# Kernel tuning notes

Hardware: AMD Instinct MI355X
Metric: run time of the kernel (lower is better)

The kernel has to match this reference:

```python
import jax, jax.numpy as jnp
import numpy as np

B, T, D, H, NC = 128, 784, 1, 512, 10


def setup_inputs() -> dict:
    key = jax.random.key(0)
    ks = jax.random.split(key, 8)
    x = jax.random.normal(ks[0], (B, T, D), dtype=jnp.float32)
    # UR-LSTM gate weights: chunks [f, r, u, o] each of size H
    Wx = jax.random.normal(ks[1], (D, 4 * H), dtype=jnp.float32) / np.sqrt(D)
    Wh = jax.random.normal(ks[2], (H, 4 * H), dtype=jnp.float32) / np.sqrt(H)
    b = jnp.zeros((4 * H,), dtype=jnp.float32)
    W1 = jax.random.normal(ks[3], (H * T, 256), dtype=jnp.float32) / np.sqrt(H * T)
    b1 = jnp.zeros((256,), dtype=jnp.float32)
    W2 = jax.random.normal(ks[4], (256, NC), dtype=jnp.float32) / np.sqrt(256)
    b2 = jnp.zeros((NC,), dtype=jnp.float32)
    return {"x": x, "Wx": Wx, "Wh": Wh, "b": b, "W1": W1, "b1": b1, "W2": W2, "b2": b2}


def _ur_lstm(x, Wx, Wh, b):
    # x: [B, T, D] -> h sequence [B, T, H]
    Bb = x.shape[0]
    Hh = Wh.shape[0]
    xz = jnp.einsum('btd,dg->btg', x, Wx) + b  # precompute input projection [B,T,4H]

    def step(carry, xz_t):
        h, c = carry
        z = xz_t + h @ Wh  # [B, 4H]
        f, r, u, o = jnp.split(z, 4, axis=-1)
        f = jax.nn.sigmoid(f)
        r = jax.nn.sigmoid(r)
        # refine gate: g = r*(1-(1-f)^2) + (1-r)*f^2
        g = r * (1.0 - (1.0 - f) ** 2) + (1.0 - r) * f ** 2
        c = g * c + (1.0 - g) * jnp.tanh(u)
        h = jax.nn.sigmoid(o) * jnp.tanh(c)
        return (h, c), h

    h0 = jnp.zeros((Bb, Hh), dtype=x.dtype)
    c0 = jnp.zeros((Bb, Hh), dtype=x.dtype)
    (_, _), hs = jax.lax.scan(step, (h0, c0), jnp.swapaxes(xz, 0, 1))
    return jnp.swapaxes(hs, 0, 1)  # [B, T, H]


def reference(x, Wx, Wh, b, W1, b1, W2, b2):
    hs = _ur_lstm(x, Wx, Wh, b)                # [B, T, H]
    flat = hs.reshape(x.shape[0], -1)          # [B, T*H]
    hidden = jax.nn.relu(flat @ W1 + b1)       # [B, 256]
    out = hidden @ W2 + b2                     # [B, NC]
    return out
```

## Files before the change

### kernel.cpp

```cpp
#include <hip/hip_runtime.h>
#include <hip/hip_bf16.h>
#include <stdint.h>

#define B_  128
#define T_  784
#define H_  512
#define G4  2048
#define NC_ 10

#define GB 8
#define GC 32
#define NWG (GB*GC)

typedef __bf16 bf16x8 __attribute__((ext_vector_type(8)));
typedef float  f32x4  __attribute__((ext_vector_type(4)));
typedef unsigned int       u32;
typedef unsigned long long u64;

static __device__ __forceinline__ float bf2f(unsigned short u){
  union { unsigned int i; float f; } v; v.i = ((unsigned int)u) << 16; return v.f;
}
static __device__ __forceinline__ unsigned short f2bf_rn(float f){
  union { float f; unsigned int i; } v; v.f = f;
  unsigned int x = v.i;
  unsigned int lsb = (x >> 16) & 1u;
  x += 0x7fffu + lsb;
  return (unsigned short)(x >> 16);
}

static __device__ __forceinline__ float fsig(float z){
  return __builtin_amdgcn_rcpf(1.f + __expf(-z));
}
static __device__ __forceinline__ float ftanh(float z){
  return 2.f * __builtin_amdgcn_rcpf(1.f + __expf(-2.f * z)) - 1.f;
}

__global__ void prep_wh(const float* __restrict__ Wh,
                        unsigned short* __restrict__ whT_hi,
                        unsigned short* __restrict__ whT_lo){
  int idx = blockIdx.x * blockDim.x + threadIdx.x;
  int kb  = idx >> 11;
  int g   = idx & 2047;
  int k0  = kb * 8;
  unsigned short hi8[8], lo8[8];
  #pragma unroll
  for (int j = 0; j < 8; ++j){
    float v = Wh[(size_t)(k0 + j) * G4 + g];
    unsigned short hi = f2bf_rn(v);
    hi8[j] = hi;
    lo8[j] = f2bf_rn(v - bf2f(hi));
  }
  *(uint4*)(whT_hi + (size_t)g * H_ + k0) = *(const uint4*)hi8;
  *(uint4*)(whT_lo + (size_t)g * H_ + k0) = *(const uint4*)lo8;
}

__global__ __launch_bounds__(256, 1) void scan_k(
    const float* __restrict__ x, const float* __restrict__ Wx,
    const float* __restrict__ bias,
    const unsigned short* __restrict__ whT_hi,
    const unsigned short* __restrict__ whT_lo,
    u32* __restrict__ hbp,
    unsigned short* __restrict__ hs,
    u32* __restrict__ flags)
{
  const int wg  = blockIdx.x;
  const int bg  = wg & 7;
  const int cg  = wg >> 3;
  const int b0  = bg * 16;
  const int c0  = cg * 16;
  const int tid = threadIdx.x;
  const int wv  = tid >> 6;
  const int lane = tid & 63;
  const int nl  = lane & 15;
  const int kc  = lane >> 4;

  __shared__ float xs[16 * 784];
  __shared__ __align__(16) unsigned short hhi[16 * 512];
  __shared__ __align__(16) unsigned short hlo[16 * 512];
  __shared__ float zbuf[16][16][17];

  for (int i = tid; i < 16 * 784; i += 256) xs[i] = x[(size_t)b0 * 784 + i];

  bf16x8 bhi[4][4], blo[4][4];
  #pragma unroll
  for (int q = 0; q < 4; ++q){
    const int gcol = q * 512 + c0 + nl;
    const unsigned short* ph = whT_hi + (size_t)gcol * H_;
    const unsigned short* pl = whT_lo + (size_t)gcol * H_;
    #pragma unroll
    for (int kkl = 0; kkl < 4; ++kkl){
      int ko = (wv * 4 + kkl) * 32 + kc * 8;
      bhi[q][kkl] = *(const bf16x8*)(ph + ko);
      blo[q][kkl] = *(const bf16x8*)(pl + ko);
    }
  }

  const int r_  = tid >> 4;
  const int cl_ = tid & 15;
  float wx4[4], bb4[4];
  #pragma unroll
  for (int q = 0; q < 4; ++q){
    wx4[q] = Wx[q * 512 + c0 + cl_];
    bb4[q] = bias[q * 512 + c0 + cl_];
  }
  float c_st = 0.f;

  u32* const myflag = flags + (bg * 32 + cg);
  const u32* const grpflags = flags + bg * 32;

  __syncthreads();

  for (int t = 0; t < T_; ++t){
    f32x4 zq[4];
    #pragma unroll
    for (int q = 0; q < 4; ++q) zq[q] = (f32x4){0.f, 0.f, 0.f, 0.f};

    if (t > 0){
      {
        int guard = 0;
        for (;;){
          u32 v = 0xffffffffu;
          if (lane < 32)
            v = __hip_atomic_load(grpflags + lane, __ATOMIC_RELAXED, __HIP_MEMORY_SCOPE_AGENT);
          if (__all(v >= (u32)t)) break;
          if (++guard > (1 << 22)) break;
        }
        asm volatile("" ::: "memory");
      }

      const u64* hb8 = (const u64*)(hbp + (size_t)(t & 1) * B_ * H_);
      u64 vv[16];
      #pragma unroll
      for (int j = 0; j < 16; ++j)
        vv[j] = __hip_atomic_load(hb8 + (size_t)(b0 + j) * 256 + tid,
                                  __ATOMIC_RELAXED, __HIP_MEMORY_SCOPE_AGENT);
      #pragma unroll
      for (int j = 0; j < 16; ++j){
        u32 a = (u32)vv[j], b = (u32)(vv[j] >> 32);
        u32 hip_ = (a >> 16) | (b & 0xffff0000u);
        u32 lop_ = (a & 0xffffu) | (b << 16);
        int off = (4 * tid) ^ ((j & 7) << 4);
        *(u32*)((char*)hhi + j * 1024 + off) = hip_;
        *(u32*)((char*)hlo + j * 1024 + off) = lop_;
      }

      f32x4 ahh[4], ahl[4], alh[4];
      #pragma unroll
      for (int q = 0; q < 4; ++q){ ahh[q] = (f32x4){0,0,0,0}; ahl[q] = (f32x4){0,0,0,0}; alh[q] = (f32x4){0,0,0,0}; }

      const int base = nl * 1024;
      const int swz  = (nl & 7) << 4;
      #pragma unroll
      for (int kkl = 0; kkl < 4; ++kkl){
        int bo = (wv * 4 + kkl) * 64 + kc * 16;
        int ad = base + (bo ^ swz);
        bf16x8 ah = *(const bf16x8*)((const char*)hhi + ad);
        bf16x8 al = *(const bf16x8*)((const char*)hlo + ad);
        #pragma unroll
        for (int q = 0; q < 4; ++q){
          ahh[q] = __builtin_amdgcn_mfma_f32_16x16x32_bf16(ah, bhi[q][kkl], ahh[q], 0, 0, 0);
          ahl[q] = __builtin_amdgcn_mfma_f32_16x16x32_bf16(ah, blo[q][kkl], ahl[q], 0, 0, 0);
          alh[q] = __builtin_amdgcn_mfma_f32_16x16x32_bf16(al, bhi[q][kkl], alh[q], 0, 0, 0);
        }
      }
      #pragma unroll
      for (int q = 0; q < 4; ++q) zq[q] = ahh[q] + (ahl[q] + alh[q]);
    }

    #pragma unroll
    for (int q = 0; q < 4; ++q){
      #pragma unroll
      for (int i = 0; i < 4; ++i) zbuf[wv * 4 + q][kc * 4 + i][nl] = zq[q][i];
    }
    __syncthreads();

    unsigned short hi_keep;
    {
      float xv = xs[r_ * 784 + t];
      float zf = zbuf[0][r_][cl_] + zbuf[4][r_][cl_] + zbuf[8][r_][cl_]  + zbuf[12][r_][cl_] + xv * wx4[0] + bb4[0];
      float zr = zbuf[1][r_][cl_] + zbuf[5][r_][cl_] + zbuf[9][r_][cl_]  + zbuf[13][r_][cl_] + xv * wx4[1] + bb4[1];
      float zu = zbuf[2][r_][cl_] + zbuf[6][r_][cl_] + zbuf[10][r_][cl_] + zbuf[14][r_][cl_] + xv * wx4[2] + bb4[2];
      float zo = zbuf[3][r_][cl_] + zbuf[7][r_][cl_] + zbuf[11][r_][cl_] + zbuf[15][r_][cl_] + xv * wx4[3] + bb4[3];
      float f  = fsig(zf);
      float r  = fsig(zr);
      float omf = 1.f - f;
      float g  = r * (1.f - omf * omf) + (1.f - r) * (f * f);
      c_st = g * c_st + (1.f - g) * ftanh(zu);
      float h = fsig(zo) * ftanh(c_st);
      unsigned short hi = f2bf_rn(h);
      unsigned short lo = f2bf_rn(h - bf2f(hi));
      hi_keep = hi;
      u32 packed = ((u32)hi << 16) | (u32)lo;
      __hip_atomic_store(hbp + (size_t)((t + 1) & 1) * B_ * H_ +
                               (size_t)(b0 + r_) * H_ + (c0 + cl_),
                         packed, __ATOMIC_RELAXED, __HIP_MEMORY_SCOPE_AGENT);
    }

    __syncthreads();
    if (tid == 0)
      __hip_atomic_store(myflag, (u32)(t + 1), __ATOMIC_RELAXED, __HIP_MEMORY_SCOPE_AGENT);

    hs[((size_t)(b0 + r_) * T_ + t) * H_ + (c0 + cl_)] = hi_keep;
  }
}

__global__ __launch_bounds__(256, 1) void mlp1_k(
    const unsigned short* __restrict__ hs,
    const float* __restrict__ W1,
    float* __restrict__ partialT)
{
  const int cm  = blockIdx.x;
  const int tid = threadIdx.x;
  const int wv  = tid >> 6, lane = tid & 63;
  const int nl  = lane & 15, kc = lane >> 4;
  const int m_base = cm * 1568;

  f32x4 acc[4][8];
  #pragma unroll
  for (int i = 0; i < 4; ++i)
    #pragma unroll
    for (int j = 0; j < 8; ++j) acc[i][j] = (f32x4){0, 0, 0, 0};

  for (int ks = 0; ks < 49; ++ks){
    const int m0 = m_base + ks * 32 + kc * 8;
    bf16x8 bf[8];
    #pragma unroll
    for (int nt = 0; nt < 8; ++nt)
      bf[nt] = *(const bf16x8*)(hs + (size_t)(nt * 16 + nl) * 401408 + m0);

    #pragma unroll
    for (int mt = 0; mt < 4; ++mt){
      const int n = wv * 64 + mt * 16 + nl;
      union { bf16x8 v; unsigned short u[8]; } Ah, Al;
      #pragma unroll
      for (int j = 0; j < 8; ++j){
        float av = W1[(size_t)(m0 + j) * 256 + n];
        unsigned short hi = f2bf_rn(av);
        Ah.u[j] = hi;
        Al.u[j] = f2bf_rn(av - bf2f(hi));
      }
      #pragma unroll
      for (int nt = 0; nt < 8; ++nt){
        acc[mt][nt] = __builtin_amdgcn_mfma_f32_16x16x32_bf16(Ah.v, bf[nt], acc[mt][nt], 0, 0, 0);
        acc[mt][nt] = __builtin_amdgcn_mfma_f32_16x16x32_bf16(Al.v, bf[nt], acc[mt][nt], 0, 0, 0);
      }
    }
  }

  #pragma unroll
  for (int mt = 0; mt < 4; ++mt){
    const int n = wv * 64 + mt * 16 + kc * 4;
    #pragma unroll
    for (int nt = 0; nt < 8; ++nt){
      const int b = nt * 16 + nl;
      #pragma unroll
      for (int i = 0; i < 4; ++i)
        partialT[((size_t)cm * 256 + (n + i)) * 128 + b] = acc[mt][nt][i];
    }
  }
}

__global__ void mlp2_k(const float* __restrict__ partialT,
                       const float* __restrict__ b1,
                       float* __restrict__ hiddenT){
  const int n = blockIdx.x;
  const int b = threadIdx.x;
  float s = 0.f;
  for (int cm = 0; cm < 256; ++cm)
    s += partialT[((size_t)cm * 256 + n) * 128 + b];
  s += b1[n];
  hiddenT[n * 128 + b] = s > 0.f ? s : 0.f;
}

__global__ void mlp3_k(const float* __restrict__ hiddenT,
                       const float* __restrict__ W2,
                       const float* __restrict__ b2,
                       float* __restrict__ out){
  const int tid = threadIdx.x;
  for (int oi = tid; oi < B_ * NC_; oi += 256){
    int b = oi / NC_, j = oi % NC_;
    float s = b2[j];
    for (int n = 0; n < 256; ++n)
      s += hiddenT[n * 128 + b] * W2[n * NC_ + j];
    out[oi] = s;
  }
}

extern "C" void kernel_launch(void* const* d_in, const int* in_sizes, int n_in,
                              void* d_out, int out_size, void* d_ws, size_t ws_size,
                              hipStream_t stream){
  const float* x  = (const float*)d_in[0];
  const float* Wx = (const float*)d_in[1];
  const float* Wh = (const float*)d_in[2];
  const float* b  = (const float*)d_in[3];
  const float* W1 = (const float*)d_in[4];
  const float* b1 = (const float*)d_in[5];
  const float* W2 = (const float*)d_in[6];
  const float* b2 = (const float*)d_in[7];

  char* ws = (char*)d_ws;
  size_t o = 0;
  u32*            flags   = (u32*)(ws + o);            o += 1024;
  unsigned short* whT_hi  = (unsigned short*)(ws + o); o += (size_t)G4 * H_ * 2;
  unsigned short* whT_lo  = (unsigned short*)(ws + o); o += (size_t)G4 * H_ * 2;
  u32*            hbp     = (u32*)(ws + o);            o += (size_t)2 * B_ * H_ * 4;
  unsigned short* hs      = (unsigned short*)(ws + o); o += (size_t)B_ * T_ * H_ * 2;
  float*          partialT= (float*)(ws + o);          o += (size_t)256 * 256 * 128 * 4;
  float*          hiddenT = (float*)(ws + o);          o += (size_t)256 * 128 * 4;

  hipMemsetAsync(flags, 0, 1024, stream);
  hipLaunchKernelGGL(prep_wh, dim3(512), dim3(256), 0, stream, Wh, whT_hi, whT_lo);
  hipLaunchKernelGGL(scan_k,  dim3(NWG), dim3(256), 0, stream,
                     x, Wx, b, whT_hi, whT_lo, hbp, hs, flags);
  hipLaunchKernelGGL(mlp1_k,  dim3(256), dim3(256), 0, stream, hs, W1, partialT);
  hipLaunchKernelGGL(mlp2_k,  dim3(256), dim3(128), 0, stream, partialT, b1, hiddenT);
  hipLaunchKernelGGL(mlp3_k,  dim3(1),   dim3(256), 0, stream, hiddenT, W2, b2, (float*)d_out);
}
```

Measured before the change: 2.243 ms.

## Fuse first MLP layer into recurrent scan and merge head kernels

Folds the flat @ W1 projection into the scan kernel. Each workgroup multiplies its 16x16 h tile by the matching W1 slice every timestep with MFMA and accumulates in registers, and the W1 rows for the next step are prefetched into registers through a double-buffered LDS stage. This removes the large hs write/read round trip and the separate mlp1/mlp2/mlp3 kernels, replacing them with a small per-batch head kernel. In exchange it adds per-step work inside the latency-bound recurrent loop: W1 streaming, bf16 hi/lo splitting and extra MFMAs, which may lengthen the critical path of each step.

```diff
diff --git a/kernel.cpp b/kernel.cpp
--- a/kernel.cpp
+++ b/kernel.cpp
@@ -59,8 +59,9 @@
     const float* __restrict__ bias,
     const unsigned short* __restrict__ whT_hi,
     const unsigned short* __restrict__ whT_lo,
+    const float* __restrict__ W1,
     u32* __restrict__ hbp,
-    unsigned short* __restrict__ hs,
+    float* __restrict__ partialC,
     u32* __restrict__ flags)
 {
   const int wg  = blockIdx.x;
@@ -78,6 +79,10 @@
   __shared__ __align__(16) unsigned short hhi[16 * 512];
   __shared__ __align__(16) unsigned short hlo[16 * 512];
   __shared__ float zbuf[16][16][17];
+  __shared__ __align__(16) float w1f32[2][16][256];
+  __shared__ __align__(16) unsigned short w1bh[256][24];
+  __shared__ __align__(16) unsigned short w1bl[256][24];
+  __shared__ __align__(16) unsigned short htile[16][16];
 
   for (int i = tid; i < 16 * 784; i += 256) xs[i] = x[(size_t)b0 * 784 + i];
 
@@ -105,12 +110,31 @@
   }
   float c_st = 0.f;
 
+  f32x4 macc[4];
+  #pragma unroll
+  for (int m = 0; m < 4; ++m) macc[m] = (f32x4){0.f, 0.f, 0.f, 0.f};
+
   u32* const myflag = flags + (bg * 32 + cg);
   const u32* const grpflags = flags + bg * 32;
 
+  uint4 w1regs[4];
+  {
+    const char* wb = (const char*)(W1 + (size_t)c0 * 256);
+    #pragma unroll
+    for (int p = 0; p < 4; ++p)
+      w1regs[p] = *(const uint4*)(wb + (size_t)(tid + p * 256) * 16);
+  }
+
   __syncthreads();
 
   for (int t = 0; t < T_; ++t){
+    {
+      char* wdst = (char*)&w1f32[t & 1][0][0];
+      #pragma unroll
+      for (int p = 0; p < 4; ++p)
+        *(uint4*)(wdst + (size_t)(tid + p * 256) * 16) = w1regs[p];
+    }
+
     f32x4 zq[4];
     #pragma unroll
     for (int q = 0; q < 4; ++q) zq[q] = (f32x4){0.f, 0.f, 0.f, 0.f};
@@ -174,7 +198,6 @@
     }
     __syncthreads();
 
-    unsigned short hi_keep;
     {
       float xv = xs[r_ * 784 + t];
       float zf = zbuf[0][r_][cl_] + zbuf[4][r_][cl_] + zbuf[8][r_][cl_]  + zbuf[12][r_][cl_] + xv * wx4[0] + bb4[0];
@@ -189,100 +212,94 @@
       float h = fsig(zo) * ftanh(c_st);
       unsigned short hi = f2bf_rn(h);
       unsigned short lo = f2bf_rn(h - bf2f(hi));
-      hi_keep = hi;
       u32 packed = ((u32)hi << 16) | (u32)lo;
       __hip_atomic_store(hbp + (size_t)((t + 1) & 1) * B_ * H_ +
                                (size_t)(b0 + r_) * H_ + (c0 + cl_),
                          packed, __ATOMIC_RELAXED, __HIP_MEMORY_SCOPE_AGENT);
+      htile[r_][cl_] = hi;
     }
 
     __syncthreads();
     if (tid == 0)
       __hip_atomic_store(myflag, (u32)(t + 1), __ATOMIC_RELAXED, __HIP_MEMORY_SCOPE_AGENT);
 
-    hs[((size_t)(b0 + r_) * T_ + t) * H_ + (c0 + cl_)] = hi_keep;
-  }
-}
-
-__global__ __launch_bounds__(256, 1) void mlp1_k(
-    const unsigned short* __restrict__ hs,
-    const float* __restrict__ W1,
-    float* __restrict__ partialT)
-{
-  const int cm  = blockIdx.x;
-  const int tid = threadIdx.x;
-  const int wv  = tid >> 6, lane = tid & 63;
-  const int nl  = lane & 15, kc = lane >> 4;
-  const int m_base = cm * 1568;
-
-  f32x4 acc[4][8];
-  #pragma unroll
-  for (int i = 0; i < 4; ++i)
-    #pragma unroll
-    for (int j = 0; j < 8; ++j) acc[i][j] = (f32x4){0, 0, 0, 0};
-
-  for (int ks = 0; ks < 49; ++ks){
-    const int m0 = m_base + ks * 32 + kc * 8;
-    bf16x8 bf[8];
-    #pragma unroll
-    for (int nt = 0; nt < 8; ++nt)
-      bf[nt] = *(const bf16x8*)(hs + (size_t)(nt * 16 + nl) * 401408 + m0);
-
-    #pragma unroll
-    for (int mt = 0; mt < 4; ++mt){
-      const int n = wv * 64 + mt * 16 + nl;
-      union { bf16x8 v; unsigned short u[8]; } Ah, Al;
-      #pragma unroll
-      for (int j = 0; j < 8; ++j){
-        float av = W1[(size_t)(m0 + j) * 256 + n];
-        unsigned short hi = f2bf_rn(av);
-        Ah.u[j] = hi;
-        Al.u[j] = f2bf_rn(av - bf2f(hi));
-      }
-      #pragma unroll
-      for (int nt = 0; nt < 8; ++nt){
-        acc[mt][nt] = __builtin_amdgcn_mfma_f32_16x16x32_bf16(Ah.v, bf[nt], acc[mt][nt], 0, 0, 0);
-        acc[mt][nt] = __builtin_amdgcn_mfma_f32_16x16x32_bf16(Al.v, bf[nt], acc[mt][nt], 0, 0, 0);
-      }
-    }
-  }
-
-  #pragma unroll
-  for (int mt = 0; mt < 4; ++mt){
-    const int n = wv * 64 + mt * 16 + kc * 4;
-    #pragma unroll
-    for (int nt = 0; nt < 8; ++nt){
-      const int b = nt * 16 + nl;
-      #pragma unroll
-      for (int i = 0; i < 4; ++i)
-        partialT[((size_t)cm * 256 + (n + i)) * 128 + b] = acc[mt][nt][i];
-    }
-  }
-}
-
-__global__ void mlp2_k(const float* __restrict__ partialT,
+    {
+      const int nn = wv * 64 + lane;
+      const float* wsrc = &w1f32[t & 1][0][nn];
+      u32 hw[8], lw[8];
+      #pragma unroll
+      for (int i2 = 0; i2 < 8; ++i2){
+        float v0 = wsrc[(2 * i2) * 256];
+        float v1 = wsrc[(2 * i2 + 1) * 256];
+        u32 h2;
+        asm("v_cvt_pk_bf16_f32 %0, %1, %2" : "=v"(h2) : "v"(v0), "v"(v1));
+        float r0 = v0 - bf2f((unsigned short)(h2 & 0xffffu));
+        float r1 = v1 - bf2f((unsigned short)(h2 >> 16));
+        u32 l2;
+        asm("v_cvt_pk_bf16_f32 %0, %1, %2" : "=v"(l2) : "v"(r0), "v"(r1));
+        hw[i2] = h2; lw[i2] = l2;
+      }
+      *(uint4*)&w1bh[nn][0] = (uint4){hw[0], hw[1], hw[2], hw[3]};
+      *(uint4*)&w1bh[nn][8] = (uint4){hw[4], hw[5], hw[6], hw[7]};
+      *(uint4*)&w1bl[nn][0] = (uint4){lw[0], lw[1], lw[2], lw[3]};
+      *(uint4*)&w1bl[nn][8] = (uint4){lw[4], lw[5], lw[6], lw[7]};
+    }
+
+    {
+      union { u32 w[4]; bf16x8 v; } uz;
+      uz.w[0] = uz.w[1] = uz.w[2] = uz.w[3] = 0;
+      bf16x8 af = uz.v;
+      if (kc < 2) af = *(const bf16x8*)((const char*)htile + nl * 32 + kc * 16);
+      #pragma unroll
+      for (int m = 0; m < 4; ++m){
+        const int n = wv * 64 + m * 16 + nl;
+        bf16x8 bh = uz.v, bl = uz.v;
+        if (kc < 2){
+          bh = *(const bf16x8*)((const char*)w1bh + n * 48 + kc * 16);
+          bl = *(const bf16x8*)((const char*)w1bl + n * 48 + kc * 16);
+        }
+        macc[m] = __builtin_amdgcn_mfma_f32_16x16x32_bf16(af, bh, macc[m], 0, 0, 0);
+        macc[m] = __builtin_amdgcn_mfma_f32_16x16x32_bf16(af, bl, macc[m], 0, 0, 0);
+      }
+    }
+
+    if (t + 1 < T_){
+      const char* wb = (const char*)(W1 + ((size_t)(t + 1) * 512 + c0) * 256);
+      #pragma unroll
+      for (int p = 0; p < 4; ++p)
+        w1regs[p] = *(const uint4*)(wb + (size_t)(tid + p * 256) * 16);
+    }
+  }
+
+  #pragma unroll
+  for (int m = 0; m < 4; ++m){
+    const int n = wv * 64 + m * 16 + nl;
+    #pragma unroll
+    for (int i = 0; i < 4; ++i){
+      const int brow = kc * 4 + i;
+      partialC[((size_t)cg * 128 + b0 + brow) * 256 + n] = macc[m][i];
+    }
+  }
+}
+
+__global__ void head_k(const float* __restrict__ partialC,
                        const float* __restrict__ b1,
-                       float* __restrict__ hiddenT){
-  const int n = blockIdx.x;
-  const int b = threadIdx.x;
-  float s = 0.f;
-  for (int cm = 0; cm < 256; ++cm)
-    s += partialT[((size_t)cm * 256 + n) * 128 + b];
-  s += b1[n];
-  hiddenT[n * 128 + b] = s > 0.f ? s : 0.f;
-}
-
-__global__ void mlp3_k(const float* __restrict__ hiddenT,
                        const float* __restrict__ W2,
                        const float* __restrict__ b2,
                        float* __restrict__ out){
-  const int tid = threadIdx.x;
-  for (int oi = tid; oi < B_ * NC_; oi += 256){
-    int b = oi / NC_, j = oi % NC_;
-    float s = b2[j];
-    for (int n = 0; n < 256; ++n)
-      s += hiddenT[n * 128 + b] * W2[n * NC_ + j];
-    out[oi] = s;
+  const int b = blockIdx.x;
+  const int n = threadIdx.x;
+  __shared__ float hl[256];
+  float s = b1[n];
+  for (int cg = 0; cg < 32; ++cg)
+    s += partialC[((size_t)cg * 128 + b) * 256 + n];
+  hl[n] = s > 0.f ? s : 0.f;
+  __syncthreads();
+  if (n < NC_){
+    float o = b2[n];
+    for (int k = 0; k < 256; ++k)
+      o += hl[k] * W2[k * NC_ + n];
+    out[b * NC_ + n] = o;
   }
 }
 
@@ -304,15 +321,12 @@
   unsigned short* whT_hi  = (unsigned short*)(ws + o); o += (size_t)G4 * H_ * 2;
   unsigned short* whT_lo  = (unsigned short*)(ws + o); o += (size_t)G4 * H_ * 2;
   u32*            hbp     = (u32*)(ws + o);            o += (size_t)2 * B_ * H_ * 4;
-  unsigned short* hs      = (unsigned short*)(ws + o); o += (size_t)B_ * T_ * H_ * 2;
-  float*          partialT= (float*)(ws + o);          o += (size_t)256 * 256 * 128 * 4;
-  float*          hiddenT = (float*)(ws + o);          o += (size_t)256 * 128 * 4;
+  float*          partialC= (float*)(ws + o);          o += (size_t)32 * B_ * 256 * 4;
 
   hipMemsetAsync(flags, 0, 1024, stream);
   hipLaunchKernelGGL(prep_wh, dim3(512), dim3(256), 0, stream, Wh, whT_hi, whT_lo);
   hipLaunchKernelGGL(scan_k,  dim3(NWG), dim3(256), 0, stream,
-                     x, Wx, b, whT_hi, whT_lo, hbp, hs, flags);
-  hipLaunchKernelGGL(mlp1_k,  dim3(256), dim3(256), 0, stream, hs, W1, partialT);
-  hipLaunchKernelGGL(mlp2_k,  dim3(256), dim3(128), 0, stream, partialT, b1, hiddenT);
-  hipLaunchKernelGGL(mlp3_k,  dim3(1),   dim3(256), 0, stream, hiddenT, W2, b2, (float*)d_out);
-}
+                     x, Wx, b, whT_hi, whT_lo, W1, hbp, partialC, flags);
+  hipLaunchKernelGGL(head_k,  dim3(B_),  dim3(256), 0, stream,
+                     partialC, b1, W2, b2, (float*)d_out);
+}
```

Measured after the change: 3.074 ms. 1.37x slower.

## Replace per-step block barrier with per-wave atomic flag increments and double-buffered zbuf

Applied to the files above, without the earlier changes.

Removes the second __syncthreads per timestep. Each wave now waits on its own stores with s_waitcnt and atomically increments the workgroup flag, so consumers wait for a count of 4*t instead of t. zbuf is double-buffered by step parity so the next step's writes cannot race with slower waves still reading the current buffer. The spin loop also issues two flag loads per iteration and halves the guard limit. The trade-off is four atomic RMWs per workgroup per step instead of one store, plus added ordering subtleties around the hs store and the flag update.

```diff
diff --git a/kernel.cpp b/kernel.cpp
--- a/kernel.cpp
+++ b/kernel.cpp
@@ -77,7 +77,7 @@
   __shared__ float xs[16 * 784];
   __shared__ __align__(16) unsigned short hhi[16 * 512];
   __shared__ __align__(16) unsigned short hlo[16 * 512];
-  __shared__ float zbuf[16][16][17];
+  __shared__ float zbuf[2][16][16][17];
 
   for (int i = tid; i < 16 * 784; i += 256) xs[i] = x[(size_t)b0 * 784 + i];
 
@@ -111,24 +111,29 @@
   __syncthreads();
 
   for (int t = 0; t < T_; ++t){
+    const int par = t & 1;
     f32x4 zq[4];
     #pragma unroll
     for (int q = 0; q < 4; ++q) zq[q] = (f32x4){0.f, 0.f, 0.f, 0.f};
 
     if (t > 0){
       {
+        const u32 tgt = 4u * (u32)t;
         int guard = 0;
         for (;;){
-          u32 v = 0xffffffffu;
-          if (lane < 32)
-            v = __hip_atomic_load(grpflags + lane, __ATOMIC_RELAXED, __HIP_MEMORY_SCOPE_AGENT);
-          if (__all(v >= (u32)t)) break;
-          if (++guard > (1 << 22)) break;
+          u32 v1 = 0xffffffffu, v2 = 0xffffffffu;
+          if (lane < 32){
+            v1 = __hip_atomic_load(grpflags + lane, __ATOMIC_RELAXED, __HIP_MEMORY_SCOPE_AGENT);
+            v2 = __hip_atomic_load(grpflags + lane, __ATOMIC_RELAXED, __HIP_MEMORY_SCOPE_AGENT);
+          }
+          if (__all(v1 >= tgt)) break;
+          if (__all(v2 >= tgt)) break;
+          if (++guard > (1 << 21)) break;
         }
         asm volatile("" ::: "memory");
       }
 
-      const u64* hb8 = (const u64*)(hbp + (size_t)(t & 1) * B_ * H_);
+      const u64* hb8 = (const u64*)(hbp + (size_t)par * B_ * H_);
       u64 vv[16];
       #pragma unroll
       for (int j = 0; j < 16; ++j)
@@ -170,17 +175,17 @@
     #pragma unroll
     for (int q = 0; q < 4; ++q){
       #pragma unroll
-      for (int i = 0; i < 4; ++i) zbuf[wv * 4 + q][kc * 4 + i][nl] = zq[q][i];
+      for (int i = 0; i < 4; ++i) zbuf[par][wv * 4 + q][kc * 4 + i][nl] = zq[q][i];
     }
     __syncthreads();
 
     unsigned short hi_keep;
     {
       float xv = xs[r_ * 784 + t];
-      float zf = zbuf[0][r_][cl_] + zbuf[4][r_][cl_] + zbuf[8][r_][cl_]  + zbuf[12][r_][cl_] + xv * wx4[0] + bb4[0];
-      float zr = zbuf[1][r_][cl_] + zbuf[5][r_][cl_] + zbuf[9][r_][cl_]  + zbuf[13][r_][cl_] + xv * wx4[1] + bb4[1];
-      float zu = zbuf[2][r_][cl_] + zbuf[6][r_][cl_] + zbuf[10][r_][cl_] + zbuf[14][r_][cl_] + xv * wx4[2] + bb4[2];
-      float zo = zbuf[3][r_][cl_] + zbuf[7][r_][cl_] + zbuf[11][r_][cl_] + zbuf[15][r_][cl_] + xv * wx4[3] + bb4[3];
+      float zf = zbuf[par][0][r_][cl_] + zbuf[par][4][r_][cl_] + zbuf[par][8][r_][cl_]  + zbuf[par][12][r_][cl_] + xv * wx4[0] + bb4[0];
+      float zr = zbuf[par][1][r_][cl_] + zbuf[par][5][r_][cl_] + zbuf[par][9][r_][cl_]  + zbuf[par][13][r_][cl_] + xv * wx4[1] + bb4[1];
+      float zu = zbuf[par][2][r_][cl_] + zbuf[par][6][r_][cl_] + zbuf[par][10][r_][cl_] + zbuf[par][14][r_][cl_] + xv * wx4[2] + bb4[2];
+      float zo = zbuf[par][3][r_][cl_] + zbuf[par][7][r_][cl_] + zbuf[par][11][r_][cl_] + zbuf[par][15][r_][cl_] + xv * wx4[3] + bb4[3];
       float f  = fsig(zf);
       float r  = fsig(zr);
       float omf = 1.f - f;
@@ -196,9 +201,9 @@
                          packed, __ATOMIC_RELAXED, __HIP_MEMORY_SCOPE_AGENT);
     }
 
-    __syncthreads();
-    if (tid == 0)
-      __hip_atomic_store(myflag, (u32)(t + 1), __ATOMIC_RELAXED, __HIP_MEMORY_SCOPE_AGENT);
+    asm volatile("s_waitcnt vmcnt(0)" ::: "memory");
+    if (lane == 0)
+      __hip_atomic_fetch_add(myflag, 1u, __ATOMIC_RELAXED, __HIP_MEMORY_SCOPE_AGENT);
 
     hs[((size_t)(b0 + r_) * T_ + t) * H_ + (c0 + cl_)] = hi_keep;
   }
```

After: 4.513 ms. +101.2%, slower.
